# Performance work log

Hardware: AMD Instinct MI355X
Metric: run time of the kernel (lower is better)

Reference implementation:

```python
import jax, jax.numpy as jnp
import numpy as np

B, N_ROWS, N_COLS, CTRL = 16384, 2048, 128, 1024
EPS = 1e-16


def setup_inputs() -> dict:
    key = jax.random.key(0)
    k1, k2, k3 = jax.random.split(key, 3)
    x = jax.random.normal(k1, (B, CTRL), dtype=jnp.float32)
    W_fc = jax.random.normal(k2, (CTRL, N_COLS + 6), dtype=jnp.float32) * 0.02
    b_fc = jnp.zeros((N_COLS + 6,), dtype=jnp.float32)
    M = jax.random.normal(k3, (N_ROWS, N_COLS), dtype=jnp.float32)
    # initial weighting: softmax of bias with w_bias[0]=100 -> ~one-hot at row 0
    w_bias = jnp.zeros((N_ROWS,), dtype=jnp.float32).at[0].set(100.0)
    w_prev = jnp.broadcast_to(jax.nn.softmax(w_bias), (B, N_ROWS))
    return {"x": x, "W_fc": W_fc, "b_fc": b_fc, "M": M, "w_prev": w_prev}


def reference(x, W_fc, b_fc, M, w_prev):
    # dense projection + split
    h = x @ W_fc + b_fc                      # [B, N_COLS+6]
    k = h[:, :N_COLS]                        # [B, N_COLS]
    beta = jax.nn.softplus(h[:, N_COLS:N_COLS + 1])          # [B, 1]
    g = jax.nn.sigmoid(h[:, N_COLS + 1:N_COLS + 2])          # [B, 1]
    s = jax.nn.softmax(h[:, N_COLS + 2:N_COLS + 5], axis=-1) # [B, 3]
    gamma = 1.0 + jax.nn.softplus(h[:, N_COLS + 5:N_COLS + 6])  # [B, 1]

    # content addressing: cosine similarity against every memory row
    k_norm = jnp.linalg.norm(k, axis=-1, keepdims=True)       # [B, 1]
    M_norm = jnp.linalg.norm(M, axis=-1)                      # [N_ROWS]
    sim = (k @ M.T) / (k_norm * M_norm[None, :] + EPS)        # [B, N_ROWS]
    w_c = jax.nn.softmax(beta * sim, axis=-1)

    # interpolation gate
    w_g = g * w_c + (1.0 - g) * w_prev

    # circular shift convolution (shifts -1, 0, +1)
    w_tilde = (s[:, 0:1] * jnp.roll(w_g, 1, axis=1)
               + s[:, 1:2] * w_g
               + s[:, 2:3] * jnp.roll(w_g, -1, axis=1))

    # sharpening
    w_pow = (w_tilde + EPS) ** gamma
    w = w_pow / jnp.sum(w_pow, axis=-1, keepdims=True)

    # weighted read
    r = w @ M                                                 # [B, N_COLS]
    return r
```

## Files before the change

kernel.cpp:

```cpp
#include <hip/hip_runtime.h>
#include <hip/hip_bf16.h>

#define NB    16384
#define NR    2048
#define NC    128
#define KCTRL 1024
#define EPSF  1e-16f
#define ESTR  2056
#define XSTR  1032

typedef __attribute__((ext_vector_type(8))) short bf16x8;
typedef __attribute__((ext_vector_type(4))) float f32x4;

__device__ __forceinline__ float softplus_f(float x) {
    return fmaxf(x, 0.f) + log1pf(__expf(-fabsf(x)));
}
__device__ __forceinline__ unsigned short f2bf(float f) {
    __hip_bfloat16 h = __float2bfloat16(f);
    return *(unsigned short*)&h;
}
__device__ __forceinline__ float bf2f(unsigned short u) {
    __hip_bfloat16 h;
    *(unsigned short*)&h = u;
    return __bfloat162float(h);
}

__device__ __forceinline__ size_t swz(int n, int k, int nch) {
    return ((size_t)((n >> 4) * nch + (k >> 5)) * 64 + ((k >> 3) & 3) * 16 + (n & 15)) * 8 + (k & 7);
}

__global__ __launch_bounds__(64) void prep_all(const float* __restrict__ M,
                                               unsigned short* __restrict__ Mb_sw,
                                               unsigned short* __restrict__ Mt_sw,
                                               float* __restrict__ imn,
                                               const float* __restrict__ W,
                                               unsigned short* __restrict__ Wt_sw) {
    const int bid = blockIdx.x;
    const int l = threadIdx.x;
    if (bid < NR) {
        const int i = bid;
        const float v0 = M[(size_t)i * NC + l];
        const float v1 = M[(size_t)i * NC + 64 + l];
        Mb_sw[swz(i, l, 4)]      = f2bf(v0);
        Mb_sw[swz(i, 64 + l, 4)] = f2bf(v1);
        Mt_sw[swz(l, i, 64)]      = f2bf(v0);
        Mt_sw[swz(64 + l, i, 64)] = f2bf(v1);
        float s = v0 * v0 + v1 * v1;
        #pragma unroll
        for (int m = 1; m < 64; m <<= 1) s += __shfl_xor(s, m);
        if (l == 0) imn[i] = 1.f / sqrtf(s);
    } else {
        const int k = bid - NR;
        Wt_sw[swz(l, k, 32)]      = f2bf(W[(size_t)k * 134 + l]);
        Wt_sw[swz(64 + l, k, 32)] = f2bf(W[(size_t)k * 134 + 64 + l]);
        if (l < 6) {
            Wt_sw[swz(128 + l, k, 32)] = f2bf(W[(size_t)k * 134 + 128 + l]);
        }
    }
}

__global__ __launch_bounds__(256, 3) void fc_mfma(const float* __restrict__ x,
                                                  const unsigned short* __restrict__ Wt_sw,
                                                  const float* __restrict__ bfc,
                                                  unsigned short* __restrict__ k_sw,
                                                  float* __restrict__ scal) {
    __shared__ __align__(16) char smem[4 * 16 * 148 * 4];
    __shared__ float kv[16][132];
    __shared__ float h6s[16][6];

    unsigned short (*x_s)[XSTR] = (unsigned short(*)[XSTR])smem;
    float (*red)[16][148] = (float(*)[16][148])smem;

    const int tid  = threadIdx.x;
    const int w    = tid >> 6;
    const int lane = tid & 63;
    const int quad = lane >> 4;
    const int l16  = lane & 15;
    const int b0   = blockIdx.x * 16;

    #pragma unroll
    for (int p = 0; p < 16; p++) {
        const int idx = p * 256 + tid;
        const int row = idx >> 8;
        const int c4  = idx & 255;
        const float4 v = *(const float4*)(x + (size_t)(b0 + row) * KCTRL + c4 * 4);
        unsigned short* d = &x_s[row][c4 * 4];
        d[0] = f2bf(v.x); d[1] = f2bf(v.y); d[2] = f2bf(v.z); d[3] = f2bf(v.w);
    }
    __syncthreads();

    bf16x8 A[8];
    #pragma unroll
    for (int i = 0; i < 8; i++) {
        A[i] = *(const bf16x8*)&x_s[l16][w * 256 + i * 32 + quad * 8];
    }

    f32x4 acc[9];
    #pragma unroll
    for (int t = 0; t < 9; t++) acc[t] = (f32x4){0.f, 0.f, 0.f, 0.f};
    const unsigned short* wb = Wt_sw + (size_t)(w * 8) * 512 + lane * 8;
    #pragma unroll
    for (int t = 0; t < 9; t++) {
        const unsigned short* wt = wb + (size_t)t * 32 * 512;
        #pragma unroll
        for (int i = 0; i < 8; i++) {
            const bf16x8 bf = *(const bf16x8*)(wt + i * 512);
            acc[t] = __builtin_amdgcn_mfma_f32_16x16x32_bf16(A[i], bf, acc[t], 0, 0, 0);
        }
    }
    __syncthreads();

    #pragma unroll
    for (int t = 0; t < 9; t++) {
        #pragma unroll
        for (int reg = 0; reg < 4; reg++) {
            red[w][quad * 4 + reg][t * 16 + l16] = acc[t][reg];
        }
    }
    __syncthreads();

    #pragma unroll
    for (int e = 0; e < 9; e++) {
        const int f = tid + 256 * e;
        const int m = f / 144;
        const int c = f - m * 144;
        const float v = red[0][m][c] + red[1][m][c] + red[2][m][c] + red[3][m][c] + bfc[c];
        if (c < 128) {
            k_sw[(size_t)(b0 >> 4) * 2048 + swz(m, c, 4)] = f2bf(v);
            kv[m][c] = v;
        } else if (c < 134) {
            h6s[m][c - 128] = v;
        }
    }
    __syncthreads();

    {
        const int m = tid >> 4;
        const int l = tid & 15;
        float s = 0.f;
        #pragma unroll
        for (int i = 0; i < 8; i++) {
            const float v = kv[m][l + 16 * i];
            s = fmaf(v, v, s);
        }
        #pragma unroll
        for (int ss = 1; ss < 16; ss <<= 1) s += __shfl_xor(s, ss);
        if (l == 0) {
            const float kn = sqrtf(s);
            const float* h = h6s[m];
            const float beta = softplus_f(h[0]);
            const float g = 1.f / (1.f + __expf(-h[1]));
            const float m3 = fmaxf(h[2], fmaxf(h[3], h[4]));
            const float e0 = __expf(h[2] - m3), e1 = __expf(h[3] - m3), e2 = __expf(h[4] - m3);
            const float inv = 1.f / (e0 + e1 + e2);
            const float gamma = 1.f + softplus_f(h[5]);
            float* sc = scal + (size_t)(b0 + m) * 8;
            sc[0] = beta / kn; sc[1] = g; sc[2] = e0 * inv; sc[3] = e1 * inv;
            sc[4] = e2 * inv; sc[5] = gamma; sc[6] = 0.f; sc[7] = 0.f;
        }
    }
}

__global__ __launch_bounds__(512, 4) void head_mfma(const unsigned short* __restrict__ Mb_sw,
                                                    const unsigned short* __restrict__ Mt_sw,
                                                    const float* __restrict__ imn,
                                                    const unsigned short* __restrict__ k_sw,
                                                    const float* __restrict__ scal,
                                                    const float* __restrict__ wprev,
                                                    float* __restrict__ out) {
    __shared__ __align__(16) unsigned short E_s[16][ESTR];
    __shared__ float scal_s[16][8];
    __shared__ float wred[16][8];
    __shared__ float fa_s[16], fc_s[16], invZ_s[16];

    const int tid  = threadIdx.x;
    const int w    = tid >> 6;
    const int lane = tid & 63;
    const int quad = lane >> 4;
    const int l16  = lane & 15;
    const int b0   = blockIdx.x * 16;

    if (tid < 128) scal_s[tid >> 3][tid & 7] = scal[(size_t)(b0 + (tid >> 3)) * 8 + (tid & 7)];
    __syncthreads();

    float cbs[4];
    #pragma unroll
    for (int reg = 0; reg < 4; reg++) cbs[reg] = scal_s[quad * 4 + reg][0];

    const unsigned short* ks = k_sw + (size_t)blockIdx.x * 2048 + lane * 8;
    const bf16x8 af0 = *(const bf16x8*)(ks);
    const bf16x8 af1 = *(const bf16x8*)(ks + 512);
    const bf16x8 af2 = *(const bf16x8*)(ks + 1024);
    const bf16x8 af3 = *(const bf16x8*)(ks + 1536);

    float Sp[4] = {0.f, 0.f, 0.f, 0.f};
    #pragma unroll 4
    for (int t = 0; t < 16; t++) {
        const int nt = w * 16 + t;
        const unsigned short* bp = Mb_sw + (size_t)nt * 2048 + lane * 8;
        f32x4 aA = {0.f, 0.f, 0.f, 0.f};
        f32x4 aB = {0.f, 0.f, 0.f, 0.f};
        aA = __builtin_amdgcn_mfma_f32_16x16x32_bf16(af0, *(const bf16x8*)(bp), aA, 0, 0, 0);
        aB = __builtin_amdgcn_mfma_f32_16x16x32_bf16(af2, *(const bf16x8*)(bp + 1024), aB, 0, 0, 0);
        aA = __builtin_amdgcn_mfma_f32_16x16x32_bf16(af1, *(const bf16x8*)(bp + 512), aA, 0, 0, 0);
        aB = __builtin_amdgcn_mfma_f32_16x16x32_bf16(af3, *(const bf16x8*)(bp + 1536), aB, 0, 0, 0);
        const int n0 = nt * 16;
        const float im = imn[n0 + l16];
        #pragma unroll
        for (int reg = 0; reg < 4; reg++) {
            const float e = __expf((aA[reg] + aB[reg]) * cbs[reg] * im);
            E_s[quad * 4 + reg][n0 + l16] = f2bf(e);
            Sp[reg] += e;
        }
    }
    #pragma unroll
    for (int s = 1; s < 16; s <<= 1) {
        #pragma unroll
        for (int reg = 0; reg < 4; reg++) Sp[reg] += __shfl_xor(Sp[reg], s);
    }
    if (l16 == 0) {
        #pragma unroll
        for (int reg = 0; reg < 4; reg++) wred[quad * 4 + reg][w] = Sp[reg];
    }
    __syncthreads();
    if (tid < 16) {
        float S = 0.f;
        #pragma unroll
        for (int i = 0; i < 8; i++) S += wred[tid][i];
        const float g = scal_s[tid][1];
        fa_s[tid] = g / S;
        fc_s[tid] = 1.f - g;
    }
    __syncthreads();

    {
        const int row  = tid >> 5;
        const int g    = tid & 31;
        const int base = tid & 32;
        const float s0 = scal_s[row][2], s1 = scal_s[row][3], s2 = scal_s[row][4];
        const float gmm = scal_s[row][5];
        const float fa = fa_s[row], fcm = fc_s[row];
        const float* wp = wprev + (size_t)(b0 + row) * NR;

        float Zp = 0.f;
        float carry = 0.f, E0sav = 0.f;
        #pragma unroll
        for (int j = 0; j < 8; j++) {
            const int c0 = (g + 32 * j) * 8;
            const bf16x8 E8 = *(const bf16x8*)&E_s[row][c0];
            float ef[8];
            #pragma unroll
            for (int i = 0; i < 8; i++) ef[i] = bf2f((unsigned short)E8[i]);
            const float eLraw = bf2f(E_s[row][(c0 + NR - 1) & (NR - 1)]);
            const float eRraw = bf2f(E_s[row][(c0 + 8) & (NR - 1)]);
            if (j == 0) E0sav = __shfl(ef[0], base);
            const float eL = (g == 0 && j > 0) ? carry : eLraw;
            const float eR = (g == 31 && j == 7) ? E0sav : eRraw;
            carry = __shfl(ef[7], base + 31);

            const float4 wa = *(const float4*)(wp + c0);
            const float4 wb = *(const float4*)(wp + c0 + 4);
            const float wpL = wp[(c0 + NR - 1) & (NR - 1)];
            const float wpR = wp[(c0 + 8) & (NR - 1)];

            float wg[10];
            wg[0] = fmaf(fa, eL,    fcm * wpL);
            wg[1] = fmaf(fa, ef[0], fcm * wa.x);
            wg[2] = fmaf(fa, ef[1], fcm * wa.y);
            wg[3] = fmaf(fa, ef[2], fcm * wa.z);
            wg[4] = fmaf(fa, ef[3], fcm * wa.w);
            wg[5] = fmaf(fa, ef[4], fcm * wb.x);
            wg[6] = fmaf(fa, ef[5], fcm * wb.y);
            wg[7] = fmaf(fa, ef[6], fcm * wb.z);
            wg[8] = fmaf(fa, ef[7], fcm * wb.w);
            wg[9] = fmaf(fa, eR,    fcm * wpR);

            bf16x8 out8;
            #pragma unroll
            for (int i = 0; i < 8; i++) {
                const float wt = fmaf(s0, wg[i], fmaf(s1, wg[i + 1], s2 * wg[i + 2])) + EPSF;
                const float pw = __expf(gmm * __logf(wt));
                Zp += pw;
                out8[i] = (short)f2bf(pw);
            }
            *(bf16x8*)&E_s[row][c0] = out8;
        }
        #pragma unroll
        for (int s = 1; s < 32; s <<= 1) Zp += __shfl_xor(Zp, s);
        if (g == 0) invZ_s[row] = 1.f / Zp;
    }
    __syncthreads();

    {
        f32x4 acc0 = {0.f, 0.f, 0.f, 0.f};
        f32x4 acc1 = {0.f, 0.f, 0.f, 0.f};
        f32x4 acc2 = {0.f, 0.f, 0.f, 0.f};
        f32x4 acc3 = {0.f, 0.f, 0.f, 0.f};
        const unsigned short* bp = Mt_sw + (size_t)w * 32768 + lane * 8;
        for (int k0 = 0; k0 < NR; k0 += 128) {
            const int C = k0 >> 5;
            const bf16x8 a0 = *(const bf16x8*)&E_s[l16][k0 + quad * 8];
            const bf16x8 a1 = *(const bf16x8*)&E_s[l16][k0 + 32 + quad * 8];
            const bf16x8 a2 = *(const bf16x8*)&E_s[l16][k0 + 64 + quad * 8];
            const bf16x8 a3 = *(const bf16x8*)&E_s[l16][k0 + 96 + quad * 8];
            const bf16x8 b0v = *(const bf16x8*)(bp + (size_t)C * 512);
            const bf16x8 b1v = *(const bf16x8*)(bp + (size_t)(C + 1) * 512);
            const bf16x8 b2v = *(const bf16x8*)(bp + (size_t)(C + 2) * 512);
            const bf16x8 b3v = *(const bf16x8*)(bp + (size_t)(C + 3) * 512);
            acc0 = __builtin_amdgcn_mfma_f32_16x16x32_bf16(a0, b0v, acc0, 0, 0, 0);
            acc1 = __builtin_amdgcn_mfma_f32_16x16x32_bf16(a1, b1v, acc1, 0, 0, 0);
            acc2 = __builtin_amdgcn_mfma_f32_16x16x32_bf16(a2, b2v, acc2, 0, 0, 0);
            acc3 = __builtin_amdgcn_mfma_f32_16x16x32_bf16(a3, b3v, acc3, 0, 0, 0);
        }
        #pragma unroll
        for (int reg = 0; reg < 4; reg++) {
            const int m = quad * 4 + reg;
            const float v = (acc0[reg] + acc1[reg]) + (acc2[reg] + acc3[reg]);
            out[(size_t)(b0 + m) * NC + w * 16 + l16] = v * invZ_s[m];
        }
    }
}

extern "C" void kernel_launch(void* const* d_in, const int* in_sizes, int n_in,
                              void* d_out, int out_size, void* d_ws, size_t ws_size,
                              hipStream_t stream) {
    const float* x     = (const float*)d_in[0];
    const float* Wfc   = (const float*)d_in[1];
    const float* bfc   = (const float*)d_in[2];
    const float* M     = (const float*)d_in[3];
    const float* wprev = (const float*)d_in[4];
    float* out = (float*)d_out;

    char* ws = (char*)d_ws;
    unsigned short* k_sw  = (unsigned short*)(ws);
    float*          scal  = (float*)(ws + 4194304);
    float*          imn   = (float*)(ws + 4718592);
    unsigned short* Mb_sw = (unsigned short*)(ws + 4726784);
    unsigned short* Mt_sw = (unsigned short*)(ws + 5251072);
    unsigned short* Wt_sw = (unsigned short*)(ws + 5775360);

    hipLaunchKernelGGL(prep_all, dim3(NR + KCTRL), dim3(64), 0, stream,
                       M, Mb_sw, Mt_sw, imn, Wfc, Wt_sw);
    hipLaunchKernelGGL(fc_mfma, dim3(NB / 16), dim3(256), 0, stream, x, Wt_sw, bfc, k_sw, scal);
    hipLaunchKernelGGL(head_mfma, dim3(NB / 16), dim3(512), 0, stream,
                       Mb_sw, Mt_sw, imn, k_sw, scal, wprev, out);
}
```

Baseline: 303.8 us.

## Fuse FC projection into head kernel, keeping k and scalars in LDS

Merges the fc_mfma and head_mfma kernels into one fused_ntm kernel. The projected key k and the per-row scalars now stay in shared memory instead of going through global workspace buffers. The FC GEMM is re-split so each of 8 waves owns one 16-column N-tile across the full K dimension, with wave 0 also computing the 6 extra head columns. Row norms are summed through LDS atomics. This removes a kernel launch and a global round trip, but wave 0 does extra work and the x staging reuses the E_s buffer.

```diff
diff --git a/kernel.cpp b/kernel.cpp
--- a/kernel.cpp
+++ b/kernel.cpp
@@ -59,17 +59,23 @@
     }
 }
 
-__global__ __launch_bounds__(256, 3) void fc_mfma(const float* __restrict__ x,
-                                                  const unsigned short* __restrict__ Wt_sw,
-                                                  const float* __restrict__ bfc,
-                                                  unsigned short* __restrict__ k_sw,
-                                                  float* __restrict__ scal) {
-    __shared__ __align__(16) char smem[4 * 16 * 148 * 4];
-    __shared__ float kv[16][132];
+__global__ __launch_bounds__(512, 4) void fused_ntm(const float* __restrict__ x,
+                                                    const unsigned short* __restrict__ Wt_sw,
+                                                    const float* __restrict__ bfc,
+                                                    const unsigned short* __restrict__ Mb_sw,
+                                                    const unsigned short* __restrict__ Mt_sw,
+                                                    const float* __restrict__ imn,
+                                                    const float* __restrict__ wprev,
+                                                    float* __restrict__ out) {
+    __shared__ __align__(16) unsigned short E_s[16][ESTR];
+    __shared__ __align__(16) unsigned short k_s[16][136];
     __shared__ float h6s[16][6];
-
-    unsigned short (*x_s)[XSTR] = (unsigned short(*)[XSTR])smem;
-    float (*red)[16][148] = (float(*)[16][148])smem;
+    __shared__ float ksum[16];
+    __shared__ float scal_s[16][6];
+    __shared__ float wred[16][8];
+    __shared__ float fa_s[16], fc_s[16], invZ_s[16];
+
+    unsigned short (*x_s)[XSTR] = (unsigned short(*)[XSTR])E_s;
 
     const int tid  = threadIdx.x;
     const int w    = tid >> 6;
@@ -78,9 +84,10 @@
     const int l16  = lane & 15;
     const int b0   = blockIdx.x * 16;
 
+    if (tid < 16) ksum[tid] = 0.f;
     #pragma unroll
-    for (int p = 0; p < 16; p++) {
-        const int idx = p * 256 + tid;
+    for (int p = 0; p < 8; p++) {
+        const int idx = p * 512 + tid;
         const int row = idx >> 8;
         const int c4  = idx & 255;
         const float4 v = *(const float4*)(x + (size_t)(b0 + row) * KCTRL + c4 * 4);
@@ -89,138 +96,105 @@
     }
     __syncthreads();
 
-    bf16x8 A[8];
-    #pragma unroll
-    for (int i = 0; i < 8; i++) {
-        A[i] = *(const bf16x8*)&x_s[l16][w * 256 + i * 32 + quad * 8];
-    }
-
-    f32x4 acc[9];
-    #pragma unroll
-    for (int t = 0; t < 9; t++) acc[t] = (f32x4){0.f, 0.f, 0.f, 0.f};
-    const unsigned short* wb = Wt_sw + (size_t)(w * 8) * 512 + lane * 8;
-    #pragma unroll
-    for (int t = 0; t < 9; t++) {
-        const unsigned short* wt = wb + (size_t)t * 32 * 512;
-        #pragma unroll
-        for (int i = 0; i < 8; i++) {
-            const bf16x8 bf = *(const bf16x8*)(wt + i * 512);
-            acc[t] = __builtin_amdgcn_mfma_f32_16x16x32_bf16(A[i], bf, acc[t], 0, 0, 0);
-        }
-    }
-    __syncthreads();
-
-    #pragma unroll
-    for (int t = 0; t < 9; t++) {
+    {
+        f32x4 accF = {0.f, 0.f, 0.f, 0.f};
+        f32x4 accH = {0.f, 0.f, 0.f, 0.f};
+        const unsigned short* wbp = Wt_sw + (size_t)w * 32 * 512 + lane * 8;
+        const unsigned short* whp = Wt_sw + (size_t)8 * 32 * 512 + lane * 8;
+        #pragma unroll 4
+        for (int i = 0; i < 32; i++) {
+            const bf16x8 a = *(const bf16x8*)&x_s[l16][i * 32 + quad * 8];
+            const bf16x8 b = *(const bf16x8*)(wbp + (size_t)i * 512);
+            accF = __builtin_amdgcn_mfma_f32_16x16x32_bf16(a, b, accF, 0, 0, 0);
+            if (w == 0) {
+                const bf16x8 bh = *(const bf16x8*)(whp + (size_t)i * 512);
+                accH = __builtin_amdgcn_mfma_f32_16x16x32_bf16(a, bh, accH, 0, 0, 0);
+            }
+        }
+        __syncthreads();
+
+        const float bb = bfc[w * 16 + l16];
+        float part[4];
         #pragma unroll
         for (int reg = 0; reg < 4; reg++) {
-            red[w][quad * 4 + reg][t * 16 + l16] = acc[t][reg];
-        }
-    }
-    __syncthreads();
-
-    #pragma unroll
-    for (int e = 0; e < 9; e++) {
-        const int f = tid + 256 * e;
-        const int m = f / 144;
-        const int c = f - m * 144;
-        const float v = red[0][m][c] + red[1][m][c] + red[2][m][c] + red[3][m][c] + bfc[c];
-        if (c < 128) {
-            k_sw[(size_t)(b0 >> 4) * 2048 + swz(m, c, 4)] = f2bf(v);
-            kv[m][c] = v;
-        } else if (c < 134) {
-            h6s[m][c - 128] = v;
-        }
+            const int m = quad * 4 + reg;
+            const float v = accF[reg] + bb;
+            k_s[m][w * 16 + l16] = f2bf(v);
+            part[reg] = v * v;
+        }
+        #pragma unroll
+        for (int s = 1; s < 16; s <<= 1) {
+            #pragma unroll
+            for (int reg = 0; reg < 4; reg++) part[reg] += __shfl_xor(part[reg], s);
+        }
+        if (l16 == 0) {
+            #pragma unroll
+            for (int reg = 0; reg < 4; reg++) atomicAdd(&ksum[quad * 4 + reg], part[reg]);
+        }
+        if (w == 0 && l16 < 6) {
+            const float bh = bfc[128 + l16];
+            #pragma unroll
+            for (int reg = 0; reg < 4; reg++) h6s[quad * 4 + reg][l16] = accH[reg] + bh;
+        }
+    }
+    __syncthreads();
+
+    if (tid < 16) {
+        const float kn = sqrtf(ksum[tid]);
+        const float* h = h6s[tid];
+        const float beta = softplus_f(h[0]);
+        const float g = 1.f / (1.f + __expf(-h[1]));
+        const float m3 = fmaxf(h[2], fmaxf(h[3], h[4]));
+        const float e0 = __expf(h[2] - m3), e1 = __expf(h[3] - m3), e2 = __expf(h[4] - m3);
+        const float inv = 1.f / (e0 + e1 + e2);
+        scal_s[tid][0] = beta / kn;
+        scal_s[tid][1] = g;
+        scal_s[tid][2] = e0 * inv;
+        scal_s[tid][3] = e1 * inv;
+        scal_s[tid][4] = e2 * inv;
+        scal_s[tid][5] = 1.f + softplus_f(h[5]);
     }
     __syncthreads();
 
     {
-        const int m = tid >> 4;
-        const int l = tid & 15;
-        float s = 0.f;
-        #pragma unroll
-        for (int i = 0; i < 8; i++) {
-            const float v = kv[m][l + 16 * i];
-            s = fmaf(v, v, s);
-        }
-        #pragma unroll
-        for (int ss = 1; ss < 16; ss <<= 1) s += __shfl_xor(s, ss);
-        if (l == 0) {
-            const float kn = sqrtf(s);
-            const float* h = h6s[m];
-            const float beta = softplus_f(h[0]);
-            const float g = 1.f / (1.f + __expf(-h[1]));
-            const float m3 = fmaxf(h[2], fmaxf(h[3], h[4]));
-            const float e0 = __expf(h[2] - m3), e1 = __expf(h[3] - m3), e2 = __expf(h[4] - m3);
-            const float inv = 1.f / (e0 + e1 + e2);
-            const float gamma = 1.f + softplus_f(h[5]);
-            float* sc = scal + (size_t)(b0 + m) * 8;
-            sc[0] = beta / kn; sc[1] = g; sc[2] = e0 * inv; sc[3] = e1 * inv;
-            sc[4] = e2 * inv; sc[5] = gamma; sc[6] = 0.f; sc[7] = 0.f;
-        }
-    }
-}
-
-__global__ __launch_bounds__(512, 4) void head_mfma(const unsigned short* __restrict__ Mb_sw,
-                                                    const unsigned short* __restrict__ Mt_sw,
-                                                    const float* __restrict__ imn,
-                                                    const unsigned short* __restrict__ k_sw,
-                                                    const float* __restrict__ scal,
-                                                    const float* __restrict__ wprev,
-                                                    float* __restrict__ out) {
-    __shared__ __align__(16) unsigned short E_s[16][ESTR];
-    __shared__ float scal_s[16][8];
-    __shared__ float wred[16][8];
-    __shared__ float fa_s[16], fc_s[16], invZ_s[16];
-
-    const int tid  = threadIdx.x;
-    const int w    = tid >> 6;
-    const int lane = tid & 63;
-    const int quad = lane >> 4;
-    const int l16  = lane & 15;
-    const int b0   = blockIdx.x * 16;
-
-    if (tid < 128) scal_s[tid >> 3][tid & 7] = scal[(size_t)(b0 + (tid >> 3)) * 8 + (tid & 7)];
-    __syncthreads();
-
-    float cbs[4];
-    #pragma unroll
-    for (int reg = 0; reg < 4; reg++) cbs[reg] = scal_s[quad * 4 + reg][0];
-
-    const unsigned short* ks = k_sw + (size_t)blockIdx.x * 2048 + lane * 8;
-    const bf16x8 af0 = *(const bf16x8*)(ks);
-    const bf16x8 af1 = *(const bf16x8*)(ks + 512);
-    const bf16x8 af2 = *(const bf16x8*)(ks + 1024);
-    const bf16x8 af3 = *(const bf16x8*)(ks + 1536);
-
-    float Sp[4] = {0.f, 0.f, 0.f, 0.f};
-    #pragma unroll 4
-    for (int t = 0; t < 16; t++) {
-        const int nt = w * 16 + t;
-        const unsigned short* bp = Mb_sw + (size_t)nt * 2048 + lane * 8;
-        f32x4 aA = {0.f, 0.f, 0.f, 0.f};
-        f32x4 aB = {0.f, 0.f, 0.f, 0.f};
-        aA = __builtin_amdgcn_mfma_f32_16x16x32_bf16(af0, *(const bf16x8*)(bp), aA, 0, 0, 0);
-        aB = __builtin_amdgcn_mfma_f32_16x16x32_bf16(af2, *(const bf16x8*)(bp + 1024), aB, 0, 0, 0);
-        aA = __builtin_amdgcn_mfma_f32_16x16x32_bf16(af1, *(const bf16x8*)(bp + 512), aA, 0, 0, 0);
-        aB = __builtin_amdgcn_mfma_f32_16x16x32_bf16(af3, *(const bf16x8*)(bp + 1536), aB, 0, 0, 0);
-        const int n0 = nt * 16;
-        const float im = imn[n0 + l16];
-        #pragma unroll
-        for (int reg = 0; reg < 4; reg++) {
-            const float e = __expf((aA[reg] + aB[reg]) * cbs[reg] * im);
-            E_s[quad * 4 + reg][n0 + l16] = f2bf(e);
-            Sp[reg] += e;
-        }
-    }
-    #pragma unroll
-    for (int s = 1; s < 16; s <<= 1) {
-        #pragma unroll
-        for (int reg = 0; reg < 4; reg++) Sp[reg] += __shfl_xor(Sp[reg], s);
-    }
-    if (l16 == 0) {
-        #pragma unroll
-        for (int reg = 0; reg < 4; reg++) wred[quad * 4 + reg][w] = Sp[reg];
+        float cbs[4];
+        #pragma unroll
+        for (int reg = 0; reg < 4; reg++) cbs[reg] = scal_s[quad * 4 + reg][0];
+
+        const bf16x8 af0 = *(const bf16x8*)&k_s[l16][quad * 8];
+        const bf16x8 af1 = *(const bf16x8*)&k_s[l16][32 + quad * 8];
+        const bf16x8 af2 = *(const bf16x8*)&k_s[l16][64 + quad * 8];
+        const bf16x8 af3 = *(const bf16x8*)&k_s[l16][96 + quad * 8];
+
+        float Sp[4] = {0.f, 0.f, 0.f, 0.f};
+        #pragma unroll 4
+        for (int t = 0; t < 16; t++) {
+            const int nt = w * 16 + t;
+            const unsigned short* bp = Mb_sw + (size_t)nt * 2048 + lane * 8;
+            f32x4 aA = {0.f, 0.f, 0.f, 0.f};
+            f32x4 aB = {0.f, 0.f, 0.f, 0.f};
+            aA = __builtin_amdgcn_mfma_f32_16x16x32_bf16(af0, *(const bf16x8*)(bp), aA, 0, 0, 0);
+            aB = __builtin_amdgcn_mfma_f32_16x16x32_bf16(af2, *(const bf16x8*)(bp + 1024), aB, 0, 0, 0);
+            aA = __builtin_amdgcn_mfma_f32_16x16x32_bf16(af1, *(const bf16x8*)(bp + 512), aA, 0, 0, 0);
+            aB = __builtin_amdgcn_mfma_f32_16x16x32_bf16(af3, *(const bf16x8*)(bp + 1536), aB, 0, 0, 0);
+            const int n0 = nt * 16;
+            const float im = imn[n0 + l16];
+            #pragma unroll
+            for (int reg = 0; reg < 4; reg++) {
+                const float e = __expf((aA[reg] + aB[reg]) * cbs[reg] * im);
+                E_s[quad * 4 + reg][n0 + l16] = f2bf(e);
+                Sp[reg] += e;
+            }
+        }
+        #pragma unroll
+        for (int s = 1; s < 16; s <<= 1) {
+            #pragma unroll
+            for (int reg = 0; reg < 4; reg++) Sp[reg] += __shfl_xor(Sp[reg], s);
+        }
+        if (l16 == 0) {
+            #pragma unroll
+            for (int reg = 0; reg < 4; reg++) wred[quad * 4 + reg][w] = Sp[reg];
+        }
     }
     __syncthreads();
     if (tid < 16) {
@@ -332,16 +306,13 @@
     float* out = (float*)d_out;
 
     char* ws = (char*)d_ws;
-    unsigned short* k_sw  = (unsigned short*)(ws);
-    float*          scal  = (float*)(ws + 4194304);
-    float*          imn   = (float*)(ws + 4718592);
-    unsigned short* Mb_sw = (unsigned short*)(ws + 4726784);
-    unsigned short* Mt_sw = (unsigned short*)(ws + 5251072);
-    unsigned short* Wt_sw = (unsigned short*)(ws + 5775360);
+    float*          imn   = (float*)(ws);
+    unsigned short* Mb_sw = (unsigned short*)(ws + 8192);
+    unsigned short* Mt_sw = (unsigned short*)(ws + 532480);
+    unsigned short* Wt_sw = (unsigned short*)(ws + 1056768);
 
     hipLaunchKernelGGL(prep_all, dim3(NR + KCTRL), dim3(64), 0, stream,
                        M, Mb_sw, Mt_sw, imn, Wfc, Wt_sw);
-    hipLaunchKernelGGL(fc_mfma, dim3(NB / 16), dim3(256), 0, stream, x, Wt_sw, bfc, k_sw, scal);
-    hipLaunchKernelGGL(head_mfma, dim3(NB / 16), dim3(512), 0, stream,
-                       Mb_sw, Mt_sw, imn, k_sw, scal, wprev, out);
-}
+    hipLaunchKernelGGL(fused_ntm, dim3(NB / 16), dim3(512), 0, stream,
+                       x, Wt_sw, bfc, Mb_sw, Mt_sw, imn, wprev, out);
+}
```

Measured after the change: 307.1 us. No clear change (+1.1%).
